# Kernel optimization log

Hardware: AMD Instinct MI355X
Metric: run time of the kernel (lower is better)

## Reference

```python
import jax, jax.numpy as jnp
import numpy as np

# Block dims (see shape_source)
D, H = 768, 12
DH = D // H            # 64 head dim
NOPE = DH // 2         # 32 non-rope q/k dim
ROPE = DH // 2         # 32 rope q/k dim
QP = D // 2            # 384 q LoRA dim
KVP = 2 * D // 3       # 512 kv LoRA dim
E, TOPK, NS = 8, 2, 2  # routed experts, top-k, shared experts
FF = 4 * D             # 3072 expert hidden
THETA = 10000.0


def setup_inputs() -> dict:
    key = jax.random.key(0)
    ks = jax.random.split(key, 16)
    B, S = 4, 1024
    r = lambda i, shape, s: (s * jax.random.normal(ks[i], shape)).astype(jnp.float32)
    return {
        'x': jax.random.normal(ks[0], (B, S, D), jnp.float32),
        'ln1_w': jnp.ones((D,), jnp.float32),
        'ln2_w': jnp.ones((D,), jnp.float32),
        'W_dq': r(1, (D, QP), 0.01),
        'W_uq': r(2, (QP, D), 0.01),
        'q_ln_w': jnp.ones((QP,), jnp.float32),
        'q_ln_b': jnp.zeros((QP,), jnp.float32),
        'W_dkv': r(3, (D, KVP + ROPE), 0.01),
        'W_ukv': r(4, (KVP, D + H * NOPE), 0.01),
        'kv_ln_w': jnp.ones((KVP,), jnp.float32),
        'kv_ln_b': jnp.zeros((KVP,), jnp.float32),
        'W_o': r(5, (D, D), 0.01),
        's_fc': r(6, (NS, FF, D), 0.02),   # nn.Linear weight layout [out,in]
        's_proj': r(7, (NS, D, FF), 0.02),
        'e_fc': r(8, (E, FF, D), 0.02),
        'e_proj': r(9, (E, D, FF), 0.02),
        'centroids': jax.random.normal(ks[10], (E, D), jnp.float32),
        'route_bias': jnp.zeros((E,), jnp.float32),  # load-balancing bias (non-learned)
    }


def _ln(x, w, b=None, eps=1e-5):
    m = x.mean(-1, keepdims=True)
    v = ((x - m) ** 2).mean(-1, keepdims=True)
    y = (x - m) * jax.lax.rsqrt(v + eps) * w
    return y + b if b is not None else y


def _rope(x, cos, sin):
    x1, x2 = jnp.split(x, 2, axis=-1)
    return x * cos + jnp.concatenate([-x2, x1], axis=-1) * sin


def _forward(x, ln1_w, ln2_w, W_dq, W_uq, q_ln_w, q_ln_b, W_dkv, W_ukv,
             kv_ln_w, kv_ln_b, W_o, s_fc, s_proj, e_fc, e_proj,
             centroids, route_bias):
    B, S, _ = x.shape
    h = _ln(x, ln1_w)
    # ---- MLA attention ----
    cq = _ln(h @ W_dq, q_ln_w, q_ln_b)
    Q = (cq @ W_uq).reshape(B, S, H, DH).transpose(0, 2, 1, 3)  # bhsd
    Qn, Qr = Q[..., :NOPE], Q[..., NOPE:]
    freqs = 1.0 / (THETA ** (jnp.arange(0, DH, 2, dtype=jnp.float32) / DH))
    ang = jnp.arange(S, dtype=jnp.float32)[:, None] * freqs[None, :]  # [S, DH/2]
    cos = jnp.tile(jnp.cos(ang)[:, : ROPE // 2], (1, 2))  # [S, ROPE]
    sin = jnp.tile(jnp.sin(ang)[:, : ROPE // 2], (1, 2))
    Qr = _rope(Qr, cos, sin)
    ckv = h @ W_dkv
    kv_lora, k_rope = ckv[..., :KVP], ckv[..., KVP:]
    kv_lora = _ln(kv_lora, kv_ln_w, kv_ln_b)
    KV = (kv_lora @ W_ukv).reshape(B, S, H, NOPE + DH).transpose(0, 2, 1, 3)
    Kn, V = KV[..., :NOPE], KV[..., NOPE:]
    Kr = _rope(k_rope[:, None, :, :], cos, sin)  # [B,1,S,ROPE] shared across heads
    Kr = jnp.broadcast_to(Kr, (B, H, S, ROPE))
    q = jnp.concatenate([Qn, Qr], axis=-1)
    k = jnp.concatenate([Kn, Kr], axis=-1)
    scores = jnp.einsum('bhsd,bhtd->bhst', q, k) / np.float32(np.sqrt(DH))
    causal = jnp.tril(jnp.ones((S, S), bool))
    scores = jnp.where(causal, scores, jnp.finfo(scores.dtype).min)
    attn = jax.nn.softmax(scores, axis=-1)
    o = jnp.einsum('bhst,bhtd->bshd', attn, V).reshape(B, S, D)
    x = x + o @ W_o.T
    # ---- MoE FFN ----
    h = _ln(x, ln2_w)
    gelu = lambda t: jax.nn.gelu(t, approximate=False)  # torch nn.GELU default
    # shared experts (always on, summed)
    shared = jnp.einsum('bsnf,ndf->bsd', gelu(jnp.einsum('bsd,nfd->bsnf', h, s_fc)), s_proj)
    # centroid routing
    raw = jnp.einsum('bsd,ed->bse', h, centroids)
    routing = jax.nn.sigmoid(raw)
    balanced = raw + route_bias
    _, topi = jax.lax.top_k(balanced, TOPK)                       # [B,S,K]
    w = jnp.take_along_axis(routing, topi, axis=-1)               # sigmoid gate values
    w = w / (w.sum(-1, keepdims=True) + 1e-9)                     # normalize over top-k
    gates = (jax.nn.one_hot(topi, E, dtype=w.dtype) * w[..., None]).sum(-2)  # [B,S,E]
    eh = gelu(jnp.einsum('bsd,efd->bsef', h, e_fc))               # [B,S,E,FF]
    routed = jnp.einsum('bsef,edf,bse->bsd', eh, e_proj, gates)
    return x + shared + routed


def reference(x, ln1_w, ln2_w, W_dq, W_uq, q_ln_w, q_ln_b, W_dkv, W_ukv,
              kv_ln_w, kv_ln_b, W_o, s_fc, s_proj, e_fc, e_proj,
              centroids, route_bias):
    return _forward(x, ln1_w, ln2_w, W_dq, W_uq, q_ln_w, q_ln_b, W_dkv, W_ukv,
                    kv_ln_w, kv_ln_b, W_o, s_fc, s_proj, e_fc, e_proj,
                    centroids, route_bias)
```

## Files before the change

kernel.cpp:

```cpp
#include <hip/hip_runtime.h>
#include <math.h>


#define DEV __device__ __forceinline__

typedef __attribute__((ext_vector_type(8))) short short8;
typedef __attribute__((ext_vector_type(8))) __bf16 bf16x8;
typedef __attribute__((ext_vector_type(4))) float floatx4;

DEV short f2bf(float f) {
  union { float f; unsigned u; } v; v.f = f;
  unsigned r = v.u + 0x7fffu + ((v.u >> 16) & 1u);
  return (short)(r >> 16);
}
DEV float bf2f(short s) {
  union { float f; unsigned u; } v; v.u = ((unsigned)(unsigned short)s) << 16;
  return v.f;
}
DEV float gelu_f(float v) {
  float z = fabsf(v) * 0.70710678118654752f;
  float t = __fdividef(1.0f, 1.0f + 0.3275911f * z);
  float poly = t * (0.254829592f + t * (-0.284496736f +
               t * (1.421413741f + t * (-1.453152027f + t * 1.061405429f))));
  float er = 1.0f - poly * __expf(-z * z);
  er = (v < 0.f) ? -er : er;
  return 0.5f * v * (1.0f + er);
}

DEV floatx4 mfma16(short8 a, short8 b, floatx4 c) {
  return __builtin_amdgcn_mfma_f32_16x16x32_bf16(
      __builtin_bit_cast(bf16x8, a), __builtin_bit_cast(bf16x8, b), c, 0, 0, 0);
}
DEV void async16(void* lds_uniform, const void* gptr) {
  __builtin_amdgcn_global_load_lds(
      (const __attribute__((address_space(1))) void*)gptr,
      (__attribute__((address_space(3))) void*)lds_uniform, 16, 0, 0);
}

DEV void xcd_swz(int& n0, int& m0) {
  const int NT = gridDim.x;
  const int flat = blockIdx.y * NT + blockIdx.x;
  const int nwg = NT * gridDim.y;
  const int w = (flat & 7) * (nwg >> 3) + (flat >> 3);
  n0 = (w % NT) * 128;
  m0 = (w / NT) * 128;
}


__global__ void cast2_bf4(const float4* __restrict__ srcA, short4* __restrict__ dstA,
                          const float4* __restrict__ srcB, short4* __restrict__ dstB,
                          long n4each) {
  long i = (long)blockIdx.x * blockDim.x + threadIdx.x;
  long stride = (long)gridDim.x * blockDim.x;
  for (; i < 2 * n4each; i += stride) {
    const float4* s; short4* d; long j;
    if (i < n4each) { s = srcA; d = dstA; j = i; }
    else { s = srcB; d = dstB; j = i - n4each; }
    float4 v = s[j];
    short4 o; o.x = f2bf(v.x); o.y = f2bf(v.y); o.z = f2bf(v.z); o.w = f2bf(v.w);
    d[j] = o;
  }
}

__global__ void cast_shared(const float4* __restrict__ sfc4, const float4* __restrict__ sproj4,
                            short4* __restrict__ fcCat4, short4* __restrict__ projCat4) {
  long i = (long)blockIdx.x * 256 + threadIdx.x;
  float4 v;
  if (i < 1179648) {
    v = sfc4[i];
    short4 o; o.x = f2bf(v.x); o.y = f2bf(v.y); o.z = f2bf(v.z); o.w = f2bf(v.w);
    fcCat4[i] = o;
  } else {
    long j = i - 1179648;
    long d = j / 1536, k4 = j - d * 1536;
    v = (k4 < 768) ? sproj4[d * 768 + k4] : sproj4[589824 + d * 768 + (k4 - 768)];
    short4 o; o.x = f2bf(v.x); o.y = f2bf(v.y); o.z = f2bf(v.z); o.w = f2bf(v.w);
    projCat4[j] = o;
  }
}

__global__ void cast_hl4(const float4* __restrict__ src, short4* __restrict__ dhi,
                         short4* __restrict__ dlo, long n4) {
  long i = (long)blockIdx.x * blockDim.x + threadIdx.x;
  long stride = (long)gridDim.x * blockDim.x;
  for (; i < n4; i += stride) {
    float4 v = src[i];
    short4 h, l;
    h.x = f2bf(v.x); l.x = f2bf(v.x - bf2f(h.x));
    h.y = f2bf(v.y); l.y = f2bf(v.y - bf2f(h.y));
    h.z = f2bf(v.z); l.z = f2bf(v.z - bf2f(h.z));
    h.w = f2bf(v.w); l.w = f2bf(v.w - bf2f(h.w));
    dhi[i] = h; dlo[i] = l;
  }
}

__launch_bounds__(256)
__global__ void transpose_cast_hl(const float* __restrict__ src, short* __restrict__ dhi,
                                  short* __restrict__ dlo, int K, int N) {
  __shared__ float tile[64][65];
  int k0 = blockIdx.x * 64, n0 = blockIdx.y * 64;
  for (int i = threadIdx.x; i < 4096; i += 256) {
    int r = i >> 6, c = i & 63;
    tile[r][c] = (n0 + c < N) ? src[(size_t)(k0 + r) * N + n0 + c] : 0.f;
  }
  __syncthreads();
  for (int i = threadIdx.x; i < 4096; i += 256) {
    int r = i >> 6, c = i & 63;
    float v = tile[c][r];
    short h = f2bf(v);
    dhi[(size_t)(n0 + r) * K + k0 + c] = h;
    dlo[(size_t)(n0 + r) * K + k0 + c] = f2bf(v - bf2f(h));
  }
}


__launch_bounds__(256)
__global__ void ln_hl(const float* __restrict__ in, int ldi, int N,
                      const float* __restrict__ w, const float* __restrict__ b,
                      short* __restrict__ ohi, short* __restrict__ olo, int ldo) {
  const int row = blockIdx.x * 4 + (threadIdx.x >> 6);
  const int lane = threadIdx.x & 63;
  const float* r = in + (size_t)row * ldi;
  float s = 0.f, s2 = 0.f;
  for (int i = lane; i < N; i += 64) { float v = r[i]; s += v; s2 += v * v; }
#pragma unroll
  for (int off = 32; off >= 1; off >>= 1) { s += __shfl_xor(s, off); s2 += __shfl_xor(s2, off); }
  float mean = s / N, var = s2 / N - mean * mean;
  float rstd = rsqrtf(var + 1e-5f);
  for (int i = lane; i < N; i += 64) {
    float y = (r[i] - mean) * rstd * w[i];
    if (b) y += b[i];
    short h = f2bf(y);
    ohi[(size_t)row * ldo + i] = h;
    olo[(size_t)row * ldo + i] = f2bf(y - bf2f(h));
  }
}

__launch_bounds__(256)
__global__ void ln_qkv(const float* __restrict__ Ccat,
                       const float* __restrict__ qw, const float* __restrict__ qb,
                       const float* __restrict__ kw, const float* __restrict__ kb,
                       short* __restrict__ cqH, short* __restrict__ cqL,
                       short* __restrict__ kvH, short* __restrict__ kvL) {
  const int vrow = blockIdx.x * 4 + (threadIdx.x >> 6);
  const int lane = threadIdx.x & 63;
  const float* r; int N; const float* w; const float* b; short* oh; short* ol; int ldo; int row;
  if (vrow < 4096) {
    row = vrow; r = Ccat + (size_t)row * 928; N = 384; w = qw; b = qb; oh = cqH; ol = cqL; ldo = 384;
  } else {
    row = vrow - 4096; r = Ccat + (size_t)row * 928 + 384; N = 512; w = kw; b = kb; oh = kvH; ol = kvL; ldo = 512;
  }
  float s = 0.f, s2 = 0.f;
  for (int i = lane; i < N; i += 64) { float v = r[i]; s += v; s2 += v * v; }
#pragma unroll
  for (int off = 32; off >= 1; off >>= 1) { s += __shfl_xor(s, off); s2 += __shfl_xor(s2, off); }
  float mean = s / N, var = s2 / N - mean * mean;
  float rstd = rsqrtf(var + 1e-5f);
  for (int i = lane; i < N; i += 64) {
    float y = (r[i] - mean) * rstd * w[i] + b[i];
    short h = f2bf(y);
    oh[(size_t)row * ldo + i] = h;
    ol[(size_t)row * ldo + i] = f2bf(y - bf2f(h));
  }
}

__launch_bounds__(256)
__global__ void ln_bf_f32(const float* __restrict__ in, const float* __restrict__ w,
                          short* __restrict__ obf, float* __restrict__ of,
                          float* __restrict__ outInit) {
  const int row = blockIdx.x * 4 + (threadIdx.x >> 6);
  const int lane = threadIdx.x & 63;
  const float* r = in + (size_t)row * 768;
  float s = 0.f, s2 = 0.f;
  for (int i = lane; i < 768; i += 64) { float v = r[i]; s += v; s2 += v * v; }
#pragma unroll
  for (int off = 32; off >= 1; off >>= 1) { s += __shfl_xor(s, off); s2 += __shfl_xor(s2, off); }
  float mean = s / 768.f, var = s2 / 768.f - mean * mean;
  float rstd = rsqrtf(var + 1e-5f);
  for (int i = lane; i < 768; i += 64) {
    float xv = r[i];
    float y = (xv - mean) * rstd * w[i];
    obf[(size_t)row * 768 + i] = f2bf(y);
    of[(size_t)row * 768 + i] = y;
    outInit[(size_t)row * 768 + i] = xv;
  }
}


template<int RESID>
__launch_bounds__(256)
__global__ void gemm3(const short* __restrict__ Ahi, const short* __restrict__ Alo, int lda,
                      const short* __restrict__ Bhi, const short* __restrict__ Blo, int ldb,
                      float* __restrict__ Cf, int ldc, const float* __restrict__ resid,
                      int M, int N, int K) {
  __shared__ __align__(16) short AsH[4096], AsL[4096], BsH[4096], BsL[4096];
  const int tid = threadIdx.x;
  int n0, m0; xcd_swz(n0, m0);
  const int wave = tid >> 6, lane = tid & 63;
  const int wm = (wave >> 1) * 64, wn = (wave & 1) * 64;
  const int lr = lane & 15, rb = (lane >> 4) * 4;
  const int stg = ((tid & 3) ^ ((tid >> 3) & 3)) * 8;
  const int lkx = (((lane >> 4) ^ ((lr >> 1) & 3))) * 8;
  const floatx4 fz = {0.f, 0.f, 0.f, 0.f};
  floatx4 acc[4][4];
#pragma unroll
  for (int i = 0; i < 4; i++)
#pragma unroll
    for (int j = 0; j < 4; j++) acc[i][j] = fz;
  const size_t rowA = (size_t)(m0 + (tid >> 2)) * lda + stg;
  const size_t rowB = (size_t)(n0 + (tid >> 2)) * ldb + stg;
  const size_t a64 = (size_t)64 * lda, b64 = (size_t)64 * ldb;
  short* AsHW = AsH + wave * 512; short* AsLW = AsL + wave * 512;
  short* BsHW = BsH + wave * 512; short* BsLW = BsL + wave * 512;
  for (int k0 = 0; k0 < K; k0 += 32) {
    async16(AsHW, Ahi + rowA + k0);        async16(AsHW + 2048, Ahi + rowA + a64 + k0);
    async16(AsLW, Alo + rowA + k0);        async16(AsLW + 2048, Alo + rowA + a64 + k0);
    async16(BsHW, Bhi + rowB + k0);        async16(BsHW + 2048, Bhi + rowB + b64 + k0);
    async16(BsLW, Blo + rowB + k0);        async16(BsLW + 2048, Blo + rowB + b64 + k0);
    __syncthreads();
    short8 ah[4], al[4], bh[4], bl[4];
#pragma unroll
    for (int i = 0; i < 4; i++) {
      ah[i] = *(const short8*)&AsH[(wm + i * 16 + lr) * 32 + lkx];
      al[i] = *(const short8*)&AsL[(wm + i * 16 + lr) * 32 + lkx];
    }
#pragma unroll
    for (int j = 0; j < 4; j++) {
      bh[j] = *(const short8*)&BsH[(wn + j * 16 + lr) * 32 + lkx];
      bl[j] = *(const short8*)&BsL[(wn + j * 16 + lr) * 32 + lkx];
    }
#pragma unroll
    for (int i = 0; i < 4; i++)
#pragma unroll
      for (int j = 0; j < 4; j++) {
        acc[i][j] = mfma16(ah[i], bh[j], acc[i][j]);
        acc[i][j] = mfma16(ah[i], bl[j], acc[i][j]);
        acc[i][j] = mfma16(al[i], bh[j], acc[i][j]);
      }
    __syncthreads();
  }
#pragma unroll
  for (int i = 0; i < 4; i++) {
    int row = m0 + wm + i * 16 + rb;
#pragma unroll
    for (int j = 0; j < 4; j++) {
      int col = n0 + wn + j * 16 + lr;
      if (col < N) {
#pragma unroll
        for (int r = 0; r < 4; r++) {
          int rr = row + r;
          if (rr < M) {
            float v = acc[i][j][r];
            if (RESID) v += resid[(size_t)rr * ldc + col];
            Cf[(size_t)rr * ldc + col] = v;
          }
        }
      }
    }
  }
}


__launch_bounds__(256)
__global__ void gemm_fc(const short* __restrict__ A, int lda,
                        const short* __restrict__ Bt, int ldb,
                        short* __restrict__ Cb, int ldc, int K) {
  __shared__ __align__(16) short As[8192], Bs[8192];
  const int tid = threadIdx.x;
  int n0, m0; xcd_swz(n0, m0);
  const int wave = tid >> 6, lane = tid & 63;
  const int wm = (wave >> 1) * 64, wn = (wave & 1) * 64;
  const int lr = lane & 15, q4 = lane >> 4, rb = q4 * 4;
  const int srow = tid >> 3;
  const int sg = ((tid & 7) ^ (srow & 7)) * 8;
  const int cx0 = ((q4 ^ (lr & 7))) * 8;
  const int cx1 = (((4 + q4) ^ (lr & 7))) * 8;
  const floatx4 fz = {0.f, 0.f, 0.f, 0.f};
  floatx4 acc[4][4];
#pragma unroll
  for (int i = 0; i < 4; i++)
#pragma unroll
    for (int j = 0; j < 4; j++) acc[i][j] = fz;
  const short* Ag = A + (size_t)(m0 + srow) * lda + sg;
  const short* Bg = Bt + (size_t)(n0 + srow) * ldb + sg;
  short* AsW = As + wave * 512; short* BsW = Bs + wave * 512;
  const size_t a32 = (size_t)32 * lda, b32 = (size_t)32 * ldb;
  for (int k0 = 0; k0 < K; k0 += 64) {
    async16(AsW,        Ag + k0);            async16(AsW + 2048, Ag + a32 + k0);
    async16(AsW + 4096, Ag + 2 * a32 + k0);  async16(AsW + 6144, Ag + 3 * a32 + k0);
    async16(BsW,        Bg + k0);            async16(BsW + 2048, Bg + b32 + k0);
    async16(BsW + 4096, Bg + 2 * b32 + k0);  async16(BsW + 6144, Bg + 3 * b32 + k0);
    __syncthreads();
#pragma unroll
    for (int ks = 0; ks < 2; ks++) {
      const int cx = ks ? cx1 : cx0;
      short8 af[4], bfr[4];
#pragma unroll
      for (int i = 0; i < 4; i++) af[i] = *(const short8*)&As[(wm + i * 16 + lr) * 64 + cx];
#pragma unroll
      for (int j = 0; j < 4; j++) bfr[j] = *(const short8*)&Bs[(wn + j * 16 + lr) * 64 + cx];
#pragma unroll
      for (int i = 0; i < 4; i++)
#pragma unroll
        for (int j = 0; j < 4; j++) acc[i][j] = mfma16(af[i], bfr[j], acc[i][j]);
    }
    __syncthreads();
  }
#pragma unroll
  for (int i = 0; i < 4; i++) {
    int row = m0 + wm + i * 16 + rb;
#pragma unroll
    for (int j = 0; j < 4; j++) {
      int col = n0 + wn + j * 16 + lr;
#pragma unroll
      for (int r = 0; r < 4; r++)
        Cb[(size_t)(row + r) * ldc + col] = f2bf(gelu_f(acc[i][j][r]));
    }
  }
}


__launch_bounds__(256)
__global__ void gemm_sk(const short* __restrict__ A, int lda,
                        const short* __restrict__ Bt, int ldb,
                        float* __restrict__ out, int ldc,
                        float* __restrict__ p1, float* __restrict__ p2, int klen) {
  __shared__ __align__(16) short As[8192], Bs[4096];
  const int tid = threadIdx.x;
  const int m0 = blockIdx.y * 128, n0 = blockIdx.x * 64;
  const int z = blockIdx.z;
  const int koff = z * klen;
  const int wave = tid >> 6, lane = tid & 63;
  const int wm = (wave >> 1) * 64, wn = (wave & 1) * 32;
  const int lr = lane & 15, q4 = lane >> 4, rb = q4 * 4;
  const int srow = tid >> 3;
  const int sg = ((tid & 7) ^ (srow & 7)) * 8;
  const int cx0 = ((q4 ^ (lr & 7))) * 8;
  const int cx1 = (((4 + q4) ^ (lr & 7))) * 8;
  const floatx4 fz = {0.f, 0.f, 0.f, 0.f};
  floatx4 acc[4][2];
#pragma unroll
  for (int i = 0; i < 4; i++)
#pragma unroll
    for (int j = 0; j < 2; j++) acc[i][j] = fz;
  const short* Ag = A + (size_t)(m0 + srow) * lda + koff + sg;
  const short* Bg = Bt + (size_t)(n0 + srow) * ldb + koff + sg;
  short* AsW = As + wave * 512; short* BsW = Bs + wave * 512;
  const size_t a32 = (size_t)32 * lda, b32 = (size_t)32 * ldb;
  for (int k0 = 0; k0 < klen; k0 += 64) {
    async16(AsW,        Ag + k0);            async16(AsW + 2048, Ag + a32 + k0);
    async16(AsW + 4096, Ag + 2 * a32 + k0);  async16(AsW + 6144, Ag + 3 * a32 + k0);
    async16(BsW,        Bg + k0);            async16(BsW + 2048, Bg + b32 + k0);
    __syncthreads();
#pragma unroll
    for (int ks = 0; ks < 2; ks++) {
      const int cx = ks ? cx1 : cx0;
      short8 af[4], bfr[2];
#pragma unroll
      for (int i = 0; i < 4; i++) af[i] = *(const short8*)&As[(wm + i * 16 + lr) * 64 + cx];
#pragma unroll
      for (int j = 0; j < 2; j++) bfr[j] = *(const short8*)&Bs[(wn + j * 16 + lr) * 64 + cx];
#pragma unroll
      for (int i = 0; i < 4; i++)
#pragma unroll
        for (int j = 0; j < 2; j++) acc[i][j] = mfma16(af[i], bfr[j], acc[i][j]);
    }
    __syncthreads();
  }
  float* dst = (z == 0) ? out : (z == 1 ? p1 : p2);
#pragma unroll
  for (int i = 0; i < 4; i++) {
    int row = m0 + wm + i * 16 + rb;
#pragma unroll
    for (int j = 0; j < 2; j++) {
      int col = n0 + wn + j * 16 + lr;
#pragma unroll
      for (int r = 0; r < 4; r++) {
        size_t idx = (size_t)(row + r) * ldc + col;
        if (z == 0) dst[idx] += acc[i][j][r];
        else dst[idx] = acc[i][j][r];
      }
    }
  }
}

__global__ void sk_reduce(float4* __restrict__ out, const float4* __restrict__ p1,
                          const float4* __restrict__ p2) {
  int i = blockIdx.x * 256 + threadIdx.x;
  const int stride = gridDim.x * 256;
  for (; i < 786432; i += stride) {
    float4 o = out[i], a = p1[i], b = p2[i];
    o.x += a.x + b.x;
    o.y += a.y + b.y;
    o.z += a.z + b.z;
    o.w += a.w + b.w;
    out[i] = o;
  }
}


__global__ void build_qk(const float* __restrict__ Qf, const float* __restrict__ KVf,
                         const float* __restrict__ Ccat,
                         short* __restrict__ qh, short* __restrict__ ql,
                         short* __restrict__ kh, short* __restrict__ kl) {
  int id = blockIdx.x * blockDim.x + threadIdx.x;
  if (id >= 4096 * 12) return;
  int token = id / 12, hh_ = id - token * 12;
  int s = token & 1023, b = token >> 10;
  size_t base = ((size_t)(b * 12 + hh_) * 1024 + s) * 64;
  float vals[64];
  if (blockIdx.y == 0) {
    const float* q = Qf + (size_t)token * 768 + hh_ * 64;
#pragma unroll
    for (int d = 0; d < 32; d++) vals[d] = q[d];
#pragma unroll
    for (int i = 0; i < 16; i++) {
      float fi = powf(10000.f, -(float)(2 * i) / 64.f);
      float sn, cs; sincosf((float)s * fi, &sn, &cs);
      vals[32 + i] = q[32 + i] * cs - q[48 + i] * sn;
      vals[48 + i] = q[48 + i] * cs + q[32 + i] * sn;
    }
#pragma unroll
    for (int d = 0; d < 64; d++) {
      short h = f2bf(vals[d]);
      qh[base + d] = h; ql[base + d] = f2bf(vals[d] - bf2f(h));
    }
  } else {
    const float* kv = KVf + (size_t)token * 1152 + hh_ * 96;
#pragma unroll
    for (int d = 0; d < 32; d++) vals[d] = kv[d];
    const float* kr = Ccat + (size_t)token * 928 + 896;
#pragma unroll
    for (int i = 0; i < 16; i++) {
      float fi = powf(10000.f, -(float)(2 * i) / 64.f);
      float sn, cs; sincosf((float)s * fi, &sn, &cs);
      vals[32 + i] = kr[i] * cs - kr[16 + i] * sn;
      vals[48 + i] = kr[16 + i] * cs + kr[i] * sn;
    }
#pragma unroll
    for (int d = 0; d < 64; d++) {
      short h = f2bf(vals[d]);
      kh[base + d] = h; kl[base + d] = f2bf(vals[d] - bf2f(h));
    }
  }
}

__launch_bounds__(256)
__global__ void build_vt_hl(const float* __restrict__ KVf,
                            short* __restrict__ vth, short* __restrict__ vtl) {
  __shared__ float tile[64][65];
  const int s0 = blockIdx.x * 64, bh = blockIdx.y;
  const int b = bh / 12, h = bh - b * 12;
  for (int i = threadIdx.x; i < 4096; i += 256) {
    int tl = i >> 6, d = i & 63;
    int token = b * 1024 + s0 + tl;
    tile[tl][d] = KVf[(size_t)token * 1152 + h * 96 + 32 + d];
  }
  __syncthreads();
  for (int i = threadIdx.x; i < 4096; i += 256) {
    int d = i >> 6, sl = i & 63;
    float v = tile[sl][d];
    short hh = f2bf(v);
    size_t idx = (size_t)bh * 65536 + (size_t)d * 1024 + s0 + sl;
    vth[idx] = hh;
    vtl[idx] = f2bf(v - bf2f(hh));
  }
}


__launch_bounds__(256)
__global__ void attn3(const short* __restrict__ qbh, const short* __restrict__ qbl,
                      const short* __restrict__ kbh, const short* __restrict__ kbl,
                      const short* __restrict__ vth, const short* __restrict__ vtl,
                      short* __restrict__ obh, short* __restrict__ obl) {
  const int bh = blockIdx.y;
  const int b = bh / 12, h = bh - b * 12;
  const short* Qh = qbh + (size_t)bh * 65536;
  const short* Ql = qbl + (size_t)bh * 65536;
  const short* Kh = kbh + (size_t)bh * 65536;
  const short* Kl = kbl + (size_t)bh * 65536;
  const short* Vh = vth + (size_t)bh * 65536;
  const short* Vl = vtl + (size_t)bh * 65536;
  __shared__ __align__(16) short KsH[4096], KsL[4096], VsH[4096], VsL[4096];
  __shared__ __align__(16) short PsH[4608], PsL[4608];
  const int tid = threadIdx.x, wave = tid >> 6, lane = tid & 63;
  const int lr = lane & 15, q4 = lane >> 4, lk = (lane >> 4) * 8;
  const int sx0 = ((q4 ^ (lr & 7))) * 8;
  const int sx1 = (((4 + q4) ^ (lr & 7))) * 8;
  const int soff_sw = (((tid & 7) ^ ((tid >> 3) & 7))) * 8;
  const int srow = tid >> 3;
  short* KsHW = KsH + wave * 512; short* KsLW = KsL + wave * 512;
  short* VsHW = VsH + wave * 512; short* VsLW = VsL + wave * 512;
  short* myPh = PsH + wave * 1152; short* myPl = PsL + wave * 1152;
  const floatx4 fz = {0.f, 0.f, 0.f, 0.f};
#pragma unroll
  for (int ph = 0; ph < 2; ph++) {
    const int qt = ph ? 15 - blockIdx.x : blockIdx.x;
    const int qrow0 = qt * 64 + wave * 16;
    short8 qfh[2], qfl[2];
    qfh[0] = *(const short8*)&Qh[(size_t)(qrow0 + lr) * 64 + lk];
    qfh[1] = *(const short8*)&Qh[(size_t)(qrow0 + lr) * 64 + 32 + lk];
    qfl[0] = *(const short8*)&Ql[(size_t)(qrow0 + lr) * 64 + lk];
    qfl[1] = *(const short8*)&Ql[(size_t)(qrow0 + lr) * 64 + 32 + lk];
    floatx4 oacc[4];
#pragma unroll
    for (int t = 0; t < 4; t++) oacc[t] = fz;
    float m_i[4], l_i[4];
#pragma unroll
    for (int r = 0; r < 4; r++) { m_i[r] = -__builtin_inff(); l_i[r] = 0.f; }
    for (int kt = 0; kt <= qt; kt++) {
      __syncthreads();
      size_t krow = (size_t)(kt * 64 + srow) * 64 + soff_sw;
      size_t vrow = (size_t)srow * 1024 + kt * 64 + soff_sw;
      async16(KsHW, Kh + krow);        async16(KsHW + 2048, Kh + krow + 32 * 64);
      async16(KsLW, Kl + krow);        async16(KsLW + 2048, Kl + krow + 32 * 64);
      async16(VsHW, Vh + vrow);        async16(VsHW + 2048, Vh + vrow + 32 * 1024);
      async16(VsLW, Vl + vrow);        async16(VsLW + 2048, Vl + vrow + 32 * 1024);
      __syncthreads();
      floatx4 sacc[4];
#pragma unroll
      for (int j = 0; j < 4; j++) sacc[j] = fz;
#pragma unroll
      for (int j = 0; j < 4; j++) {
        int rbase = (j * 16 + lr) * 64;
        short8 kh0 = *(const short8*)&KsH[rbase + sx0];
        short8 kh1 = *(const short8*)&KsH[rbase + sx1];
        short8 kl0 = *(const short8*)&KsL[rbase + sx0];
        short8 kl1 = *(const short8*)&KsL[rbase + sx1];
        sacc[j] = mfma16(qfh[0], kh0, sacc[j]);
        sacc[j] = mfma16(qfh[1], kh1, sacc[j]);
        sacc[j] = mfma16(qfh[0], kl0, sacc[j]);
        sacc[j] = mfma16(qfh[1], kl1, sacc[j]);
        sacc[j] = mfma16(qfl[0], kh0, sacc[j]);
        sacc[j] = mfma16(qfl[1], kh1, sacc[j]);
      }
      float pv[4][4], mrow[4];
#pragma unroll
      for (int r = 0; r < 4; r++) mrow[r] = -__builtin_inff();
      const bool diag = (kt == qt);
#pragma unroll
      for (int j = 0; j < 4; j++)
#pragma unroll
        for (int r = 0; r < 4; r++) {
          float v = sacc[j][r] * 0.125f;
          if (diag) {
            int qg = qrow0 + q4 * 4 + r;
            int kg = kt * 64 + j * 16 + lr;
            if (kg > qg) v = -__builtin_inff();
          }
          pv[j][r] = v;
          mrow[r] = fmaxf(mrow[r], v);
        }
#pragma unroll
      for (int r = 0; r < 4; r++)
#pragma unroll
        for (int off = 1; off < 16; off <<= 1) mrow[r] = fmaxf(mrow[r], __shfl_xor(mrow[r], off));
      float alpha[4], rsum[4];
#pragma unroll
      for (int r = 0; r < 4; r++) {
        float nm = fmaxf(m_i[r], mrow[r]);
        alpha[r] = __expf(m_i[r] - nm);
        m_i[r] = nm; rsum[r] = 0.f;
      }
#pragma unroll
      for (int j = 0; j < 4; j++)
#pragma unroll
        for (int r = 0; r < 4; r++) {
          float pe = __expf(pv[j][r] - m_i[r]);
          pv[j][r] = pe; rsum[r] += pe;
        }
#pragma unroll
      for (int r = 0; r < 4; r++) {
#pragma unroll
        for (int off = 1; off < 16; off <<= 1) rsum[r] += __shfl_xor(rsum[r], off);
        l_i[r] = l_i[r] * alpha[r] + rsum[r];
      }
#pragma unroll
      for (int t = 0; t < 4; t++)
#pragma unroll
        for (int r = 0; r < 4; r++) oacc[t][r] *= alpha[r];
#pragma unroll
      for (int j = 0; j < 4; j++)
#pragma unroll
        for (int r = 0; r < 4; r++) {
          float p = pv[j][r];
          short hh = f2bf(p);
          myPh[(q4 * 4 + r) * 72 + j * 16 + lr] = hh;
          myPl[(q4 * 4 + r) * 72 + j * 16 + lr] = f2bf(p - bf2f(hh));
        }
      __asm__ volatile("s_waitcnt lgkmcnt(0)" ::: "memory");
#pragma unroll
      for (int c = 0; c < 2; c++) {
        short8 ph_ = *(const short8*)&myPh[lr * 72 + c * 32 + lk];
        short8 pl_ = *(const short8*)&myPl[lr * 72 + c * 32 + lk];
        const int sxc = c ? sx1 : sx0;
#pragma unroll
        for (int t = 0; t < 4; t++) {
          int rbase = (t * 16 + lr) * 64;
          short8 vh = *(const short8*)&VsH[rbase + sxc];
          short8 vl = *(const short8*)&VsL[rbase + sxc];
          oacc[t] = mfma16(ph_, vh, oacc[t]);
          oacc[t] = mfma16(ph_, vl, oacc[t]);
          oacc[t] = mfma16(pl_, vh, oacc[t]);
        }
      }
    }
#pragma unroll
    for (int t = 0; t < 4; t++)
#pragma unroll
      for (int r = 0; r < 4; r++) {
        int s = qrow0 + q4 * 4 + r;
        int token = b * 1024 + s;
        float ov = oacc[t][r] / l_i[r];
        short hh = f2bf(ov);
        size_t idx = (size_t)token * 768 + h * 64 + t * 16 + lr;
        obh[idx] = hh;
        obl[idx] = f2bf(ov - bf2f(hh));
      }
  }
}


__launch_bounds__(256)
__global__ void route_score(const float* __restrict__ h2f, const float* __restrict__ cent,
                            const float* __restrict__ rbias,
                            int* __restrict__ topexp, float* __restrict__ gates) {
  const int token = blockIdx.x * 4 + (threadIdx.x >> 6);
  const int lane = threadIdx.x & 63;
  const float* hv = h2f + (size_t)token * 768;
  float hreg[12];
#pragma unroll
  for (int ii = 0; ii < 12; ii++) hreg[ii] = hv[lane + 64 * ii];
  float raw[8];
#pragma unroll
  for (int e = 0; e < 8; e++) {
    const float* cv = cent + e * 768;
    float p = 0.f;
#pragma unroll
    for (int ii = 0; ii < 12; ii++) p += hreg[ii] * cv[lane + 64 * ii];
#pragma unroll
    for (int off = 32; off >= 1; off >>= 1) p += __shfl_xor(p, off);
    raw[e] = p;
  }
  if (lane == 0) {
    float b0 = -__builtin_inff(); int i1 = 0;
#pragma unroll
    for (int e = 0; e < 8; e++) { float be = raw[e] + rbias[e]; if (be > b0) { b0 = be; i1 = e; } }
    float b1 = -__builtin_inff(); int i2 = 0;
#pragma unroll
    for (int e = 0; e < 8; e++) {
      if (e == i1) continue;
      float be = raw[e] + rbias[e];
      if (be > b1) { b1 = be; i2 = e; }
    }
    float w1 = 1.f / (1.f + expf(-raw[i1]));
    float w2 = 1.f / (1.f + expf(-raw[i2]));
    float wsum = w1 + w2 + 1e-9f;
    topexp[token] = i1;        gates[token] = w1 / wsum;
    topexp[4096 + token] = i2; gates[4096 + token] = w2 / wsum;
  }
}

__launch_bounds__(256)
__global__ void build_lists(const int* __restrict__ topexp,
                            int* __restrict__ counts, int* __restrict__ lists) {
  const int e = blockIdx.x;
  __shared__ int wave_off[4];
  const int wave = threadIdx.x >> 6, lane = threadIdx.x & 63;
  int total = 0;
  for (int c0 = 0; c0 < 8192; c0 += 256) {
    int slot = c0 + threadIdx.x;
    bool m = (topexp[slot] == e);
    unsigned long long bal = __ballot(m);
    int wcnt = __popcll(bal);
    int lpre = __popcll(bal & ((1ull << lane) - 1ull));
    if (lane == 0) wave_off[wave] = wcnt;
    __syncthreads();
    int woff = 0;
#pragma unroll
    for (int w = 0; w < 4; w++) if (w < wave) woff += wave_off[w];
    int chunk_total = wave_off[0] + wave_off[1] + wave_off[2] + wave_off[3];
    if (m) lists[e * 4096 + total + woff + lpre] = slot;
    total += chunk_total;
    __syncthreads();
  }
  if (threadIdx.x == 0) counts[e] = total;
}


__launch_bounds__(256)
__global__ void expert_fc_z(const short* __restrict__ h2bf, const short* __restrict__ wfc,
                            const int* __restrict__ lists, const int* __restrict__ counts,
                            int ebase, short* __restrict__ act) {
  const int lz = blockIdx.z, e = ebase + lz;
  const int cnt = counts[e];
  const int m0 = blockIdx.y * 128;
  if (m0 >= cnt) return;
  const int n0 = blockIdx.x * 128;
  int aoff = 0;
  for (int i = 0; i < lz; i++) aoff += counts[ebase + i];
  __shared__ __align__(16) short As[8192], Bs[8192];
  __shared__ int slots[128];
  const int tid = threadIdx.x;
  if (tid < 128) slots[tid] = lists[e * 4096 + m0 + tid];
  __syncthreads();
  const int wave = tid >> 6, lane = tid & 63;
  const int wm = (wave >> 1) * 64, wn = (wave & 1) * 64;
  const int lr = lane & 15, q4 = lane >> 4, rb = q4 * 4;
  const int srow = tid >> 3;
  const int sg = ((tid & 7) ^ (srow & 7)) * 8;
  const int cx0 = ((q4 ^ (lr & 7))) * 8;
  const int cx1 = (((4 + q4) ^ (lr & 7))) * 8;
  int tok[4];
#pragma unroll
  for (int p = 0; p < 4; p++) tok[p] = slots[p * 32 + srow] & 4095;
  const floatx4 fz = {0.f, 0.f, 0.f, 0.f};
  floatx4 acc[4][4];
#pragma unroll
  for (int i = 0; i < 4; i++)
#pragma unroll
    for (int j = 0; j < 4; j++) acc[i][j] = fz;
  const short* Ag0 = h2bf + (size_t)tok[0] * 768 + sg;
  const short* Ag1 = h2bf + (size_t)tok[1] * 768 + sg;
  const short* Ag2 = h2bf + (size_t)tok[2] * 768 + sg;
  const short* Ag3 = h2bf + (size_t)tok[3] * 768 + sg;
  const short* Bg = wfc + (size_t)lz * (3072 * 768) + (size_t)(n0 + srow) * 768 + sg;
  short* AsW = As + wave * 512; short* BsW = Bs + wave * 512;
  const size_t b32 = (size_t)32 * 768;
  for (int k0 = 0; k0 < 768; k0 += 64) {
    async16(AsW,        Ag0 + k0);           async16(AsW + 2048, Ag1 + k0);
    async16(AsW + 4096, Ag2 + k0);           async16(AsW + 6144, Ag3 + k0);
    async16(BsW,        Bg + k0);            async16(BsW + 2048, Bg + b32 + k0);
    async16(BsW + 4096, Bg + 2 * b32 + k0);  async16(BsW + 6144, Bg + 3 * b32 + k0);
    __syncthreads();
#pragma unroll
    for (int ks = 0; ks < 2; ks++) {
      const int cx = ks ? cx1 : cx0;
      short8 af[4], bfr[4];
#pragma unroll
      for (int i = 0; i < 4; i++) af[i] = *(const short8*)&As[(wm + i * 16 + lr) * 64 + cx];
#pragma unroll
      for (int j = 0; j < 4; j++) bfr[j] = *(const short8*)&Bs[(wn + j * 16 + lr) * 64 + cx];
#pragma unroll
      for (int i = 0; i < 4; i++)
#pragma unroll
        for (int j = 0; j < 4; j++) acc[i][j] = mfma16(af[i], bfr[j], acc[i][j]);
    }
    __syncthreads();
  }
#pragma unroll
  for (int i = 0; i < 4; i++) {
    int lrow = wm + i * 16 + rb;
#pragma unroll
    for (int j = 0; j < 4; j++) {
      int col = n0 + wn + j * 16 + lr;
#pragma unroll
      for (int r = 0; r < 4; r++) {
        if (m0 + lrow + r < cnt)
          act[(size_t)(aoff + m0 + lrow + r) * 3072 + col] = f2bf(gelu_f(acc[i][j][r]));
      }
    }
  }
}

__launch_bounds__(256)
__global__ void expert_proj_z(const short* __restrict__ act, const short* __restrict__ wproj,
                              const int* __restrict__ lists, const int* __restrict__ counts,
                              int ebase, const float* __restrict__ gates,
                              float* __restrict__ out) {
  const int lz = blockIdx.z >> 2, kh = blockIdx.z & 3, e = ebase + lz;
  const int cnt = counts[e];
  const int m0 = blockIdx.y * 128;
  if (m0 >= cnt) return;
  const int n0 = blockIdx.x * 128;
  int aoff = 0;
  for (int i = 0; i < lz; i++) aoff += counts[ebase + i];
  const int koff = kh * 768;
  __shared__ __align__(16) short As[8192], Bs[8192];
  __shared__ int slots[128];
  const int tid = threadIdx.x;
  if (tid < 128) slots[tid] = lists[e * 4096 + m0 + tid];
  __syncthreads();
  const int wave = tid >> 6, lane = tid & 63;
  const int wm = (wave >> 1) * 64, wn = (wave & 1) * 64;
  const int lr = lane & 15, q4 = lane >> 4, rb = q4 * 4;
  const int srow = tid >> 3;
  const int sg = ((tid & 7) ^ (srow & 7)) * 8;
  const int cx0 = ((q4 ^ (lr & 7))) * 8;
  const int cx1 = (((4 + q4) ^ (lr & 7))) * 8;
  const floatx4 fz = {0.f, 0.f, 0.f, 0.f};
  floatx4 acc[4][4];
#pragma unroll
  for (int i = 0; i < 4; i++)
#pragma unroll
    for (int j = 0; j < 4; j++) acc[i][j] = fz;
  const short* Ag = act + (size_t)(aoff + m0 + srow) * 3072 + koff + sg;
  const short* Bg = wproj + (size_t)lz * (768 * 3072) + (size_t)(n0 + srow) * 3072 + koff + sg;
  short* AsW = As + wave * 512; short* BsW = Bs + wave * 512;
  const size_t s32 = (size_t)32 * 3072;
  for (int k0 = 0; k0 < 768; k0 += 64) {
    async16(AsW,        Ag + k0);            async16(AsW + 2048, Ag + s32 + k0);
    async16(AsW + 4096, Ag + 2 * s32 + k0);  async16(AsW + 6144, Ag + 3 * s32 + k0);
    async16(BsW,        Bg + k0);            async16(BsW + 2048, Bg + s32 + k0);
    async16(BsW + 4096, Bg + 2 * s32 + k0);  async16(BsW + 6144, Bg + 3 * s32 + k0);
    __syncthreads();
#pragma unroll
    for (int ks = 0; ks < 2; ks++) {
      const int cx = ks ? cx1 : cx0;
      short8 af[4], bfr[4];
#pragma unroll
      for (int i = 0; i < 4; i++) af[i] = *(const short8*)&As[(wm + i * 16 + lr) * 64 + cx];
#pragma unroll
      for (int j = 0; j < 4; j++) bfr[j] = *(const short8*)&Bs[(wn + j * 16 + lr) * 64 + cx];
#pragma unroll
      for (int i = 0; i < 4; i++)
#pragma unroll
        for (int j = 0; j < 4; j++) acc[i][j] = mfma16(af[i], bfr[j], acc[i][j]);
    }
    __syncthreads();
  }
#pragma unroll
  for (int i = 0; i < 4; i++) {
    int lrow = wm + i * 16 + rb;
#pragma unroll
    for (int j = 0; j < 4; j++) {
      int col = n0 + wn + j * 16 + lr;
#pragma unroll
      for (int r = 0; r < 4; r++) {
        if (m0 + lrow + r < cnt) {
          int slot = slots[lrow + r];
          int token = slot & 4095;
          atomicAdd(&out[(size_t)token * 768 + col], gates[slot] * acc[i][j][r]);
        }
      }
    }
  }
}

__global__ void bad_kernel(float* out) { out[threadIdx.x] = 1e30f; }


extern "C" void kernel_launch(void* const* d_in, const int* in_sizes, int n_in,
                              void* d_out, int out_size, void* d_ws, size_t ws_size,
                              hipStream_t stream) {
  const float* x = (const float*)d_in[0];
  const float* ln1_w = (const float*)d_in[1];
  const float* ln2_w = (const float*)d_in[2];
  const float* W_dq = (const float*)d_in[3];
  const float* W_uq = (const float*)d_in[4];
  const float* q_ln_w = (const float*)d_in[5];
  const float* q_ln_b = (const float*)d_in[6];
  const float* W_dkv = (const float*)d_in[7];
  const float* W_ukv = (const float*)d_in[8];
  const float* kv_ln_w = (const float*)d_in[9];
  const float* kv_ln_b = (const float*)d_in[10];
  const float* W_o = (const float*)d_in[11];
  const float* s_fc = (const float*)d_in[12];
  const float* s_proj = (const float*)d_in[13];
  const float* e_fc = (const float*)d_in[14];
  const float* e_proj = (const float*)d_in[15];
  const float* cent = (const float*)d_in[16];
  const float* rbias = (const float*)d_in[17];
  float* out = (float*)d_out;

  char* base = (char*)d_ws;
  size_t off = 0;
  auto take = [&](size_t bytes) -> char* {
    char* r = base + off;
    off = (off + bytes + 255) & ~(size_t)255;
    return r;
  };
  short* WcatH = (short*)take(1572864);  short* WcatL = (short*)take(1572864);
  short* WuqH  = (short*)take(589824);   short* WuqL  = (short*)take(589824);
  short* WukvH = (short*)take(1179648);  short* WukvL = (short*)take(1179648);
  short* WoH   = (short*)take(1179648);  short* WoL   = (short*)take(1179648);
  float* x2    = (float*)take(12582912);
  float* gates = (float*)take(32768);
  int*   counts= (int*)take(32);
  int*   lists = (int*)take(131072);
  int*   topexp= (int*)take(32768);
  const size_t PLANE = 6291456;
  char* pool = take(4 * 2 * PLANE);
  char* R    = take(51118080);
  size_t used = off;
  if (used > ws_size) { bad_kernel<<<1, 256, 0, stream>>>(out); return; }
  char* pA = pool;
  char* pB = pool + 2 * PLANE;
  char* pC = pool + 4 * PLANE;
  char* pD = pool + 6 * PLANE;

  short* hH   = (short*)pA;            short* hL   = (short*)(pA + PLANE);
  float* Ccat = (float*)R;
  short* cqH  = (short*)pB;            short* cqL  = (short*)(pB + 3145728);
  short* kvlH = (short*)pD;            short* kvlL = (short*)(pD + 4194304);
  float* Qf   = (float*)pC;
  float* KVf  = (float*)(R + 15204352);
  short* qbH  = (short*)pD;            short* qbL  = (short*)(pD + PLANE);
  short* kbH  = (short*)pA;            short* kbL  = (short*)(pA + PLANE);
  short* vtH  = (short*)pB;            short* vtL  = (short*)(pB + PLANE);
  short* obH  = (short*)pC;            short* obL  = (short*)(pC + PLANE);
  short* h2bf    = (short*)(pD + PLANE);
  float* h2f     = (float*)pC;
  short* sfcCat  = (short*)pA;
  short* sprojCat= (short*)(pA + 9437184);
  short* actCat  = (short*)R;
  short* efcHalf = (short*)pA;
  short* eprojHalf=(short*)(pA + 18874368);
  short* eact    = (short*)R;
  float* skP1 = (float*)pC;
  float* skP2 = x2;

  cast_hl4<<<576, 256, 0, stream>>>((const float4*)W_o, (short4*)WoH, (short4*)WoL, 147456);
  transpose_cast_hl<<<dim3(12, 6), 256, 0, stream>>>(W_dq, WcatH, WcatL, 768, 384);
  transpose_cast_hl<<<dim3(12, 10), 256, 0, stream>>>(W_dkv, WcatH + (size_t)384 * 768,
                                                      WcatL + (size_t)384 * 768, 768, 544);
  transpose_cast_hl<<<dim3(6, 12), 256, 0, stream>>>(W_uq, WuqH, WuqL, 384, 768);
  transpose_cast_hl<<<dim3(8, 18), 256, 0, stream>>>(W_ukv, WukvH, WukvL, 512, 1152);

  ln_hl<<<1024, 256, 0, stream>>>(x, 768, 768, ln1_w, nullptr, hH, hL, 768);
  gemm3<0><<<dim3(8, 32), 256, 0, stream>>>(hH, hL, 768, WcatH, WcatL, 768, Ccat, 928, nullptr, 4096, 928, 768);
  ln_qkv<<<2048, 256, 0, stream>>>(Ccat, q_ln_w, q_ln_b, kv_ln_w, kv_ln_b, cqH, cqL, kvlH, kvlL);
  gemm3<0><<<dim3(6, 32), 256, 0, stream>>>(cqH, cqL, 384, WuqH, WuqL, 384, Qf, 768, nullptr, 4096, 768, 384);
  gemm3<0><<<dim3(9, 32), 256, 0, stream>>>(kvlH, kvlL, 512, WukvH, WukvL, 512, KVf, 1152, nullptr, 4096, 1152, 512);
  build_qk<<<dim3(192, 2), 256, 0, stream>>>(Qf, KVf, Ccat, qbH, qbL, kbH, kbL);
  build_vt_hl<<<dim3(16, 48), 256, 0, stream>>>(KVf, vtH, vtL);
  attn3<<<dim3(8, 48), 256, 0, stream>>>(qbH, qbL, kbH, kbL, vtH, vtL, obH, obL);
  gemm3<1><<<dim3(6, 32), 256, 0, stream>>>(obH, obL, 768, WoH, WoL, 768, x2, 768, x, 4096, 768, 768);

  ln_bf_f32<<<1024, 256, 0, stream>>>(x2, ln2_w, h2bf, h2f, out);
  route_score<<<1024, 256, 0, stream>>>(h2f, cent, rbias, topexp, gates);
  build_lists<<<8, 256, 0, stream>>>(topexp, counts, lists);

  cast_shared<<<9216, 256, 0, stream>>>((const float4*)s_fc, (const float4*)s_proj,
                                        (short4*)sfcCat, (short4*)sprojCat);
  gemm_fc<<<dim3(48, 32), 256, 0, stream>>>(h2bf, 768, sfcCat, 768, actCat, 6144, 768);
  gemm_sk<<<dim3(12, 32, 3), 256, 0, stream>>>(actCat, 6144, sprojCat, 6144, out, 768,
                                               skP1, skP2, 2048);
  sk_reduce<<<1536, 256, 0, stream>>>((float4*)out, (const float4*)skP1, (const float4*)skP2);

  for (int h = 0; h < 2; h++) {
    cast2_bf4<<<2048, 256, 0, stream>>>(
        (const float4*)(e_fc + (size_t)h * 4 * 3072 * 768), (short4*)efcHalf,
        (const float4*)(e_proj + (size_t)h * 4 * 768 * 3072), (short4*)eprojHalf, 2359296);
    expert_fc_z<<<dim3(24, 32, 4), 256, 0, stream>>>(h2bf, efcHalf, lists, counts, h * 4, eact);
    expert_proj_z<<<dim3(6, 32, 16), 256, 0, stream>>>(eact, eprojHalf, lists, counts, h * 4, gates, out);
  }
}
```

Before: 976.1 us.

## Process all experts in one launch and replace atomic scatter with a gated gather

The routed-expert stage no longer runs two halves of four experts. It now casts all eight expert fc weights, then all proj weights, into one buffer, and launches the fc and proj GEMMs once over every expert using an expert-interleaved block mapping. The proj GEMM now covers the full K=3072 per block with a 64-wide N tile, so it drops the split-K atomics. It writes bf16 per-slot outputs that a separate gather kernel combines with the gate weights into the output. This removes atomic contention and extra launches, at the cost of rounding expert outputs to bf16 and an extra pass over the routed buffer.

Result: faster. 893.2 us (-8.5%).

```diff
diff --git a/kernel.cpp b/kernel.cpp
--- a/kernel.cpp
+++ b/kernel.cpp
@@ -46,19 +46,22 @@
   m0 = (w / NT) * 128;
 }
 
-
-__global__ void cast2_bf4(const float4* __restrict__ srcA, short4* __restrict__ dstA,
-                          const float4* __restrict__ srcB, short4* __restrict__ dstB,
-                          long n4each) {
+DEV void eswz(int BN, int& e, int& m0, int& n0) {
+  const int flat = (blockIdx.z * gridDim.y + blockIdx.y) * gridDim.x + blockIdx.x;
+  e = flat & 7;
+  const int s = flat >> 3;
+  m0 = (s & 31) * 128;
+  n0 = (s >> 5) * BN;
+}
+
+
+__global__ void cast_bf(const float4* __restrict__ src, short4* __restrict__ dst, long n4) {
   long i = (long)blockIdx.x * blockDim.x + threadIdx.x;
   long stride = (long)gridDim.x * blockDim.x;
-  for (; i < 2 * n4each; i += stride) {
-    const float4* s; short4* d; long j;
-    if (i < n4each) { s = srcA; d = dstA; j = i; }
-    else { s = srcB; d = dstB; j = i - n4each; }
-    float4 v = s[j];
+  for (; i < n4; i += stride) {
+    float4 v = src[i];
     short4 o; o.x = f2bf(v.x); o.y = f2bf(v.y); o.z = f2bf(v.z); o.w = f2bf(v.w);
-    d[j] = o;
+    dst[i] = o;
   }
 }
 
@@ -691,14 +694,12 @@
 __launch_bounds__(256)
 __global__ void expert_fc_z(const short* __restrict__ h2bf, const short* __restrict__ wfc,
                             const int* __restrict__ lists, const int* __restrict__ counts,
-                            int ebase, short* __restrict__ act) {
-  const int lz = blockIdx.z, e = ebase + lz;
+                            short* __restrict__ act) {
+  int e, m0, n0; eswz(128, e, m0, n0);
   const int cnt = counts[e];
-  const int m0 = blockIdx.y * 128;
   if (m0 >= cnt) return;
-  const int n0 = blockIdx.x * 128;
   int aoff = 0;
-  for (int i = 0; i < lz; i++) aoff += counts[ebase + i];
+  for (int i = 0; i < e; i++) aoff += counts[i];
   __shared__ __align__(16) short As[8192], Bs[8192];
   __shared__ int slots[128];
   const int tid = threadIdx.x;
@@ -724,7 +725,7 @@
   const short* Ag1 = h2bf + (size_t)tok[1] * 768 + sg;
   const short* Ag2 = h2bf + (size_t)tok[2] * 768 + sg;
   const short* Ag3 = h2bf + (size_t)tok[3] * 768 + sg;
-  const short* Bg = wfc + (size_t)lz * (3072 * 768) + (size_t)(n0 + srow) * 768 + sg;
+  const short* Bg = wfc + (size_t)e * (3072 * 768) + (size_t)(n0 + srow) * 768 + sg;
   short* AsW = As + wave * 512; short* BsW = Bs + wave * 512;
   const size_t b32 = (size_t)32 * 768;
   for (int k0 = 0; k0 < 768; k0 += 64) {
@@ -764,58 +765,53 @@
 }
 
 __launch_bounds__(256)
-__global__ void expert_proj_z(const short* __restrict__ act, const short* __restrict__ wproj,
-                              const int* __restrict__ lists, const int* __restrict__ counts,
-                              int ebase, const float* __restrict__ gates,
-                              float* __restrict__ out) {
-  const int lz = blockIdx.z >> 2, kh = blockIdx.z & 3, e = ebase + lz;
+__global__ void expert_proj_one(const short* __restrict__ act, const short* __restrict__ wproj,
+                                const int* __restrict__ lists, const int* __restrict__ counts,
+                                short* __restrict__ routed) {
+  int e, m0, n0; eswz(64, e, m0, n0);
   const int cnt = counts[e];
-  const int m0 = blockIdx.y * 128;
   if (m0 >= cnt) return;
-  const int n0 = blockIdx.x * 128;
   int aoff = 0;
-  for (int i = 0; i < lz; i++) aoff += counts[ebase + i];
-  const int koff = kh * 768;
-  __shared__ __align__(16) short As[8192], Bs[8192];
+  for (int i = 0; i < e; i++) aoff += counts[i];
+  __shared__ __align__(16) short As[8192], Bs[4096];
   __shared__ int slots[128];
   const int tid = threadIdx.x;
   if (tid < 128) slots[tid] = lists[e * 4096 + m0 + tid];
   __syncthreads();
   const int wave = tid >> 6, lane = tid & 63;
-  const int wm = (wave >> 1) * 64, wn = (wave & 1) * 64;
+  const int wm = (wave >> 1) * 64, wn = (wave & 1) * 32;
   const int lr = lane & 15, q4 = lane >> 4, rb = q4 * 4;
   const int srow = tid >> 3;
   const int sg = ((tid & 7) ^ (srow & 7)) * 8;
   const int cx0 = ((q4 ^ (lr & 7))) * 8;
   const int cx1 = (((4 + q4) ^ (lr & 7))) * 8;
   const floatx4 fz = {0.f, 0.f, 0.f, 0.f};
-  floatx4 acc[4][4];
+  floatx4 acc[4][2];
 #pragma unroll
   for (int i = 0; i < 4; i++)
 #pragma unroll
-    for (int j = 0; j < 4; j++) acc[i][j] = fz;
-  const short* Ag = act + (size_t)(aoff + m0 + srow) * 3072 + koff + sg;
-  const short* Bg = wproj + (size_t)lz * (768 * 3072) + (size_t)(n0 + srow) * 3072 + koff + sg;
+    for (int j = 0; j < 2; j++) acc[i][j] = fz;
+  const short* Ag = act + (size_t)(aoff + m0 + srow) * 3072 + sg;
+  const short* Bg = wproj + (size_t)e * (768 * 3072) + (size_t)(n0 + srow) * 3072 + sg;
   short* AsW = As + wave * 512; short* BsW = Bs + wave * 512;
   const size_t s32 = (size_t)32 * 3072;
-  for (int k0 = 0; k0 < 768; k0 += 64) {
+  for (int k0 = 0; k0 < 3072; k0 += 64) {
     async16(AsW,        Ag + k0);            async16(AsW + 2048, Ag + s32 + k0);
     async16(AsW + 4096, Ag + 2 * s32 + k0);  async16(AsW + 6144, Ag + 3 * s32 + k0);
     async16(BsW,        Bg + k0);            async16(BsW + 2048, Bg + s32 + k0);
-    async16(BsW + 4096, Bg + 2 * s32 + k0);  async16(BsW + 6144, Bg + 3 * s32 + k0);
     __syncthreads();
 #pragma unroll
     for (int ks = 0; ks < 2; ks++) {
       const int cx = ks ? cx1 : cx0;
-      short8 af[4], bfr[4];
+      short8 af[4], bfr[2];
 #pragma unroll
       for (int i = 0; i < 4; i++) af[i] = *(const short8*)&As[(wm + i * 16 + lr) * 64 + cx];
 #pragma unroll
-      for (int j = 0; j < 4; j++) bfr[j] = *(const short8*)&Bs[(wn + j * 16 + lr) * 64 + cx];
+      for (int j = 0; j < 2; j++) bfr[j] = *(const short8*)&Bs[(wn + j * 16 + lr) * 64 + cx];
 #pragma unroll
       for (int i = 0; i < 4; i++)
 #pragma unroll
-        for (int j = 0; j < 4; j++) acc[i][j] = mfma16(af[i], bfr[j], acc[i][j]);
+        for (int j = 0; j < 2; j++) acc[i][j] = mfma16(af[i], bfr[j], acc[i][j]);
     }
     __syncthreads();
   }
@@ -823,18 +819,37 @@
   for (int i = 0; i < 4; i++) {
     int lrow = wm + i * 16 + rb;
 #pragma unroll
-    for (int j = 0; j < 4; j++) {
+    for (int j = 0; j < 2; j++) {
       int col = n0 + wn + j * 16 + lr;
 #pragma unroll
       for (int r = 0; r < 4; r++) {
-        if (m0 + lrow + r < cnt) {
-          int slot = slots[lrow + r];
-          int token = slot & 4095;
-          atomicAdd(&out[(size_t)token * 768 + col], gates[slot] * acc[i][j][r]);
-        }
+        if (m0 + lrow + r < cnt)
+          routed[(size_t)slots[lrow + r] * 768 + col] = f2bf(acc[i][j][r]);
       }
     }
   }
+}
+
+__global__ void gather_routed(const short* __restrict__ routed, const float* __restrict__ gates,
+                              float* __restrict__ out) {
+  int i = blockIdx.x * 256 + threadIdx.x;
+  if (i >= 393216) return;
+  int t = i / 96, c = (i - t * 96) * 8;
+  float g1 = gates[t], g2 = gates[4096 + t];
+  short8 a = *(const short8*)&routed[(size_t)t * 768 + c];
+  short8 b = *(const short8*)&routed[(size_t)(4096 + t) * 768 + c];
+  float* o = &out[(size_t)t * 768 + c];
+  float4 o0 = *(float4*)o, o1 = *(float4*)(o + 4);
+  o0.x += g1 * bf2f(a[0]) + g2 * bf2f(b[0]);
+  o0.y += g1 * bf2f(a[1]) + g2 * bf2f(b[1]);
+  o0.z += g1 * bf2f(a[2]) + g2 * bf2f(b[2]);
+  o0.w += g1 * bf2f(a[3]) + g2 * bf2f(b[3]);
+  o1.x += g1 * bf2f(a[4]) + g2 * bf2f(b[4]);
+  o1.y += g1 * bf2f(a[5]) + g2 * bf2f(b[5]);
+  o1.z += g1 * bf2f(a[6]) + g2 * bf2f(b[6]);
+  o1.w += g1 * bf2f(a[7]) + g2 * bf2f(b[7]);
+  *(float4*)o = o0;
+  *(float4*)(o + 4) = o1;
 }
 
 __global__ void bad_kernel(float* out) { out[threadIdx.x] = 1e30f; }
@@ -904,9 +919,9 @@
   short* sfcCat  = (short*)pA;
   short* sprojCat= (short*)(pA + 9437184);
   short* actCat  = (short*)R;
-  short* efcHalf = (short*)pA;
-  short* eprojHalf=(short*)(pA + 18874368);
+  short* ewAll   = (short*)pA;
   short* eact    = (short*)R;
+  short* routed  = (short*)x2;
   float* skP1 = (float*)pC;
   float* skP2 = x2;
 
@@ -938,11 +953,9 @@
                                                skP1, skP2, 2048);
   sk_reduce<<<1536, 256, 0, stream>>>((float4*)out, (const float4*)skP1, (const float4*)skP2);
 
-  for (int h = 0; h < 2; h++) {
-    cast2_bf4<<<2048, 256, 0, stream>>>(
-        (const float4*)(e_fc + (size_t)h * 4 * 3072 * 768), (short4*)efcHalf,
-        (const float4*)(e_proj + (size_t)h * 4 * 768 * 3072), (short4*)eprojHalf, 2359296);
-    expert_fc_z<<<dim3(24, 32, 4), 256, 0, stream>>>(h2bf, efcHalf, lists, counts, h * 4, eact);
-    expert_proj_z<<<dim3(6, 32, 16), 256, 0, stream>>>(eact, eprojHalf, lists, counts, h * 4, gates, out);
-  }
-}
+  cast_bf<<<8192, 256, 0, stream>>>((const float4*)e_fc, (short4*)ewAll, 4718592);
+  expert_fc_z<<<dim3(24, 32, 8), 256, 0, stream>>>(h2bf, ewAll, lists, counts, eact);
+  cast_bf<<<8192, 256, 0, stream>>>((const float4*)e_proj, (short4*)ewAll, 4718592);
+  expert_proj_one<<<dim3(12, 32, 8), 256, 0, stream>>>(eact, ewAll, lists, counts, routed);
+  gather_routed<<<1536, 256, 0, stream>>>(routed, gates, out);
+}
```
